# Kernel optimization log

Measured on AMD Instinct MI355X. Metric: run time of the kernel, lower is better.

The kernel has to match this reference:

```python
import jax, jax.numpy as jnp
import numpy as np

B, N, S, D, K = 8, 8192, 2048, 256, 3
MLP = [256, 128]
EPS = 1e-5


def setup_inputs() -> dict:
    key = jax.random.key(0)
    ks = jax.random.split(key, 12)
    inp = {
        "xyz1": jax.random.normal(ks[0], (B, N, 3), dtype=jnp.float32),
        "xyz2": jax.random.normal(ks[1], (B, S, 3), dtype=jnp.float32),
        "points1": jax.random.normal(ks[2], (B, N, D), dtype=jnp.float32),
        "points2": jax.random.normal(ks[3], (B, S, D), dtype=jnp.float32),
        # relation conv: Conv2d(4 -> 1, kernel 1x1) == linear over last dim
        "rel_w": jax.random.normal(ks[4], (4,), dtype=jnp.float32) * 0.5,
        "rel_b": jnp.zeros((), dtype=jnp.float32),
        # mlp layer 0: Conv1d(2D -> 256, k=1) + BN
        "W0": jax.random.normal(ks[5], (MLP[0], 2 * D), dtype=jnp.float32) * (1.0 / np.sqrt(2 * D)),
        "b0": jnp.zeros((MLP[0],), dtype=jnp.float32),
        "g0": jnp.ones((MLP[0],), dtype=jnp.float32),
        "be0": jnp.zeros((MLP[0],), dtype=jnp.float32),
        # mlp layer 1: Conv1d(256 -> 128, k=1) + BN
        "W1": jax.random.normal(ks[6], (MLP[1], MLP[0]), dtype=jnp.float32) * (1.0 / np.sqrt(MLP[0])),
        "b1": jnp.zeros((MLP[1],), dtype=jnp.float32),
        "g1": jnp.ones((MLP[1],), dtype=jnp.float32),
        "be1": jnp.zeros((MLP[1],), dtype=jnp.float32),
    }
    return inp


def _gather(points, idx):
    # points: [B,S,C], idx: [B,N,K] -> [B,N,K,C]
    return jax.vmap(lambda p, i: p[i])(points, idx)


def _bn_relu(x, gamma, beta):
    # training-mode BatchNorm1d over [B,N,C]: stats over (B,N), biased var
    mean = jnp.mean(x, axis=(0, 1))
    var = jnp.var(x, axis=(0, 1))
    xn = (x - mean) * jax.lax.rsqrt(var + EPS)
    return jax.nn.relu(xn * gamma + beta)


def reference(xyz1, xyz2, points1, points2, rel_w, rel_b,
              W0, b0, g0, be0, W1, b1, g1, be1):
    # pairwise squared distances [B,N,S]
    d = (jnp.sum(xyz1 ** 2, -1)[:, :, None]
         + jnp.sum(xyz2 ** 2, -1)[:, None, :]
         - 2.0 * jnp.einsum('bnc,bmc->bnm', xyz1, xyz2))
    neg_d, idx = jax.lax.top_k(-d, K)          # K smallest distances
    dists = -neg_d                              # [B,N,K]

    offset = xyz1[:, :, None, :] - _gather(xyz2, idx)        # [B,N,K,3]
    rel = jnp.concatenate([dists[..., None], offset], -1)    # [B,N,K,4]
    weight = jax.nn.sigmoid(rel @ rel_w + rel_b)              # [B,N,K]

    interp = jnp.mean(_gather(points2, idx) * weight[..., None], axis=2)  # [B,N,D]
    h = jnp.concatenate([points1, interp], axis=-1)           # [B,N,2D]

    h = _bn_relu(jnp.einsum('bnc,oc->bno', h, W0) + b0, g0, be0)
    h = _bn_relu(jnp.einsum('bnc,oc->bno', h, W1) + b1, g1, be1)
    return h  # [B,N,128]
```

## Files before the change

### kernel.cpp

```cpp
#include <hip/hip_runtime.h>
#include <stdint.h>
#include <stddef.h>

#define B_   8
#define N_   8192
#define S_   2048
#define D_   256
#define M_   (B_*N_)
#define C0_  256
#define C1_  128
#define K2D_ 512
#define TS8_ 8
#define SEG8_ (S_/TS8_)
#define SWP_ 264

typedef __attribute__((ext_vector_type(8))) short short8;
typedef __attribute__((ext_vector_type(4))) float f32x4;
typedef __attribute__((ext_vector_type(2))) float f32x2;

__device__ __forceinline__ short f2bf(float f) {
  unsigned u = __float_as_uint(f);
  u += 0x7fffu + ((u >> 16) & 1u);
  return (short)(u >> 16);
}
__device__ __forceinline__ float bf2f(short s) {
  return __uint_as_float(((unsigned)(unsigned short)s) << 16);
}

__device__ __forceinline__ void cp16(const void* g, void* l) {
  __builtin_amdgcn_global_load_lds(
      (__attribute__((address_space(1))) void*)(g),
      (__attribute__((address_space(3))) void*)(l), 16, 0, 0);
}

__global__ void convw_kernel(const float* __restrict__ W0,
                             const float* __restrict__ W1,
                             const float* __restrict__ xyz2,
                             short* __restrict__ W0b, short* __restrict__ W1b,
                             float* __restrict__ xyz2p, float* __restrict__ stats) {
  int i = blockIdx.x * 256 + threadIdx.x;
  if (blockIdx.x == 0) {
    stats[threadIdx.x] = 0.f;
    stats[256 + threadIdx.x] = 0.f;
    stats[512 + threadIdx.x] = 0.f;
  }
  if (i < C0_ * K2D_) W0b[i] = f2bf(W0[i]);
  if (i < C1_ * C0_)  W1b[i] = f2bf(W1[i]);
  if (i < B_ * S_) {
    const int b = i >> 11, s = i & (S_ - 1);
    float x = xyz2[(size_t)i * 3 + 0];
    float y = xyz2[(size_t)i * 3 + 1];
    float z = xyz2[(size_t)i * 3 + 2];
    float ss = __fadd_rn(__fadd_rn(__fmul_rn(x, x), __fmul_rn(y, y)), __fmul_rn(z, z));
    float* xw = xyz2p + (size_t)b * 4 * S_;
    xw[s] = x; xw[S_ + s] = y; xw[2 * S_ + s] = z; xw[3 * S_ + s] = ss;
  }
}

__global__ __launch_bounds__(512, 8)
void topk_kernel(const float* __restrict__ xyz1, const float* __restrict__ xyz2p,
                 const float* __restrict__ relw, const float* __restrict__ relb,
                 int* __restrict__ idx_out, float* __restrict__ w_out) {
  __shared__ float cd[TS8_][64][3];
  __shared__ int   ci[TS8_][64][3];
  const int tid  = threadIdx.x;
  const int lane = tid & 63;
  const int seg  = __builtin_amdgcn_readfirstlane(tid >> 6);
  const int b    = blockIdx.x >> 7;
  const int n    = (blockIdx.x & 127) * 64 + lane;

  const float* p = xyz1 + ((size_t)b * N_ + n) * 3;
  const float ax = p[0], ay = p[1], az = p[2];
  const float s1 = __fadd_rn(__fadd_rn(__fmul_rn(ax, ax), __fmul_rn(ay, ay)), __fmul_rn(az, az));

  const float* xw = xyz2p + (size_t)b * 4 * S_;
  const f32x2* XP = (const f32x2*)(xw)           + seg * (SEG8_ / 2);
  const f32x2* YP = (const f32x2*)(xw + S_)      + seg * (SEG8_ / 2);
  const f32x2* ZP = (const f32x2*)(xw + 2 * S_)  + seg * (SEG8_ / 2);
  const f32x2* WP = (const f32x2*)(xw + 3 * S_)  + seg * (SEG8_ / 2);

  float d0 = 3.4e38f, d1 = 3.4e38f, d2 = 3.4e38f;
  int   i0 = 0, i1 = 0, i2 = 0;
  const int sbeg = seg * SEG8_;
  {
    #pragma clang fp contract(off)
    #pragma unroll 4
    for (int pr = 0; pr < SEG8_ / 2; pr++) {
      f32x2 X = XP[pr], Y = YP[pr], Z = ZP[pr], W = WP[pr];
      f32x2 t1 = ax * X;
      f32x2 t2 = ay * Y;
      f32x2 t3 = az * Z;
      f32x2 dt = (t1 + t2) + t3;
      f32x2 e  = s1 + W;
      f32x2 m  = 2.0f * dt;
      f32x2 d  = e - m;
      const float dlo = d.x, dhi = d.y;
      if (fminf(dlo, dhi) < d2) {
        const int s = sbeg + 2 * pr;
        if (dlo < d2) {
          if (dlo < d1) {
            d2 = d1; i2 = i1;
            if (dlo < d0) { d1 = d0; i1 = i0; d0 = dlo; i0 = s; }
            else          { d1 = dlo; i1 = s; }
          } else { d2 = dlo; i2 = s; }
        }
        if (dhi < d2) {
          if (dhi < d1) {
            d2 = d1; i2 = i1;
            if (dhi < d0) { d1 = d0; i1 = i0; d0 = dhi; i0 = s + 1; }
            else          { d1 = dhi; i1 = s + 1; }
          } else { d2 = dhi; i2 = s + 1; }
        }
      }
    }
  }
  cd[seg][lane][0] = d0; cd[seg][lane][1] = d1; cd[seg][lane][2] = d2;
  ci[seg][lane][0] = i0; ci[seg][lane][1] = i1; ci[seg][lane][2] = i2;
  __syncthreads();

  if (tid < 64) {
    float m0 = 3.4e38f, m1 = 3.4e38f, m2 = 3.4e38f;
    int   j0 = 0, j1 = 0, j2 = 0;
    #pragma unroll
    for (int sg = 0; sg < TS8_; sg++) {
      #pragma unroll
      for (int k = 0; k < 3; k++) {
        float d = cd[sg][tid][k];
        int   ix = ci[sg][tid][k];
        if (d < m2) {
          if (d < m1) {
            m2 = m1; j2 = j1;
            if (d < m0) { m1 = m0; j1 = j0; m0 = d; j0 = ix; }
            else        { m1 = d;  j1 = ix; }
          } else { m2 = d; j2 = ix; }
        }
      }
    }
    const float w0r = relw[0], w1r = relw[1], w2r = relw[2], w3r = relw[3], br = relb[0];
    const size_t base = ((size_t)b * N_ + n) * 3;
    float dd[3] = {m0, m1, m2};
    int   ii[3] = {j0, j1, j2};
    #pragma unroll
    for (int k = 0; k < 3; k++) {
      const int s = ii[k];
      float ox = ax - xw[s], oy = ay - xw[S_ + s], oz = az - xw[2 * S_ + s];
      float t = dd[k] * w0r + ox * w1r + oy * w2r + oz * w3r + br;
      float w = 1.0f / (1.0f + expf(-t));
      idx_out[base + k] = s;
      w_out[base + k] = w * (1.0f / 3.0f);
    }
  }
}

__global__ __launch_bounds__(256, 2)
void gemm1_kernel(const float* __restrict__ p1, const float* __restrict__ p2,
                  const int* __restrict__ idx, const float* __restrict__ wts,
                  const short* __restrict__ Bw, const float* __restrict__ bias,
                  short* __restrict__ Cb, float* __restrict__ stats) {
  __shared__ __align__(16) short sA[128 * 32];
  __shared__ __align__(16) short sB[2][256 * 32];
  const int tid = threadIdx.x;
  const int lane = tid & 63;
  const int wave = tid >> 6;
  const int wm = wave & 1;
  const int wn = wave >> 1;
  const size_t mbase = (size_t)blockIdx.x * 128;
  const int lrow = lane >> 2;
  const int lcol = (lane & 3) * 8;

  int rowg[2]; int ia[2][3]; float wa[2][3]; const float* pbase[2];
  #pragma unroll
  for (int t = 0; t < 2; t++) {
    const int row = (int)mbase + wave * 32 + t * 16 + lrow;
    rowg[t] = row;
    pbase[t] = p2 + (size_t)(row >> 13) * S_ * D_;
    ia[t][0] = idx[row * 3 + 0]; ia[t][1] = idx[row * 3 + 1]; ia[t][2] = idx[row * 3 + 2];
    wa[t][0] = wts[row * 3 + 0]; wa[t][1] = wts[row * 3 + 1]; wa[t][2] = wts[row * 3 + 2];
  }

  f32x4 acc[4][8] = {};
  float4 v[2][6];

  #define LOAD_A(K0)                                                          \
    if ((K0) < D_) {                                                          \
      _Pragma("unroll")                                                       \
      for (int t = 0; t < 2; t++) {                                           \
        const float* src = p1 + (size_t)rowg[t] * D_ + (K0) + lcol;           \
        v[t][0] = *(const float4*)src; v[t][1] = *(const float4*)(src + 4);   \
      }                                                                       \
    } else {                                                                  \
      const int c2 = (K0) - D_ + lcol;                                        \
      _Pragma("unroll")                                                       \
      for (int t = 0; t < 2; t++) {                                           \
        const float* q0 = pbase[t] + (size_t)ia[t][0] * D_ + c2;              \
        const float* q1 = pbase[t] + (size_t)ia[t][1] * D_ + c2;              \
        const float* q2 = pbase[t] + (size_t)ia[t][2] * D_ + c2;              \
        v[t][0] = *(const float4*)q0; v[t][1] = *(const float4*)(q0 + 4);     \
        v[t][2] = *(const float4*)q1; v[t][3] = *(const float4*)(q1 + 4);     \
        v[t][4] = *(const float4*)q2; v[t][5] = *(const float4*)(q2 + 4);     \
      }                                                                       \
    }

  #define STAGE_B(K0, BUF)                                                    \
    _Pragma("unroll")                                                         \
    for (int t = 0; t < 4; t++) {                                             \
      const int r = wave * 64 + t * 16;                                       \
      cp16(Bw + (size_t)(r + lrow) * K2D_ + (K0) + lcol, &sB[BUF][r * 32]);   \
    }

  LOAD_A(0);
  STAGE_B(0, 0);

  for (int k0 = 0, it = 0; k0 < K2D_; k0 += 32, it++) {
    #pragma unroll
    for (int t = 0; t < 2; t++) {
      const int r = wave * 32 + t * 16;
      float fv[8];
      if (k0 < D_) {
        fv[0] = v[t][0].x; fv[1] = v[t][0].y; fv[2] = v[t][0].z; fv[3] = v[t][0].w;
        fv[4] = v[t][1].x; fv[5] = v[t][1].y; fv[6] = v[t][1].z; fv[7] = v[t][1].w;
      } else {
        fv[0] = wa[t][0] * v[t][0].x + wa[t][1] * v[t][2].x + wa[t][2] * v[t][4].x;
        fv[1] = wa[t][0] * v[t][0].y + wa[t][1] * v[t][2].y + wa[t][2] * v[t][4].y;
        fv[2] = wa[t][0] * v[t][0].z + wa[t][1] * v[t][2].z + wa[t][2] * v[t][4].z;
        fv[3] = wa[t][0] * v[t][0].w + wa[t][1] * v[t][2].w + wa[t][2] * v[t][4].w;
        fv[4] = wa[t][0] * v[t][1].x + wa[t][1] * v[t][3].x + wa[t][2] * v[t][5].x;
        fv[5] = wa[t][0] * v[t][1].y + wa[t][1] * v[t][3].y + wa[t][2] * v[t][5].y;
        fv[6] = wa[t][0] * v[t][1].z + wa[t][1] * v[t][3].z + wa[t][2] * v[t][5].z;
        fv[7] = wa[t][0] * v[t][1].w + wa[t][1] * v[t][3].w + wa[t][2] * v[t][5].w;
      }
      short8 o;
      #pragma unroll
      for (int e = 0; e < 8; e++) o[e] = f2bf(fv[e]);
      *(short8*)&sA[(r + lrow) * 32 + lcol] = o;
    }
    __syncthreads();

    const int kn = k0 + 32;
    if (kn < K2D_) {
      STAGE_B(kn, (it + 1) & 1);
      LOAD_A(kn);
    }

    const int mr = lane & 15;
    const int ks = (lane >> 4) * 8;
    short8 af[4], bfr[8];
    #pragma unroll
    for (int i = 0; i < 4; i++) af[i]  = *(const short8*)&sA[(wm * 64 + i * 16 + mr) * 32 + ks];
    #pragma unroll
    for (int j = 0; j < 8; j++) bfr[j] = *(const short8*)&sB[it & 1][(wn * 128 + j * 16 + mr) * 32 + ks];
    #pragma unroll
    for (int i = 0; i < 4; i++)
      #pragma unroll
      for (int j = 0; j < 8; j++)
        acc[i][j] = __builtin_amdgcn_mfma_f32_16x16x32_bf16(af[i], bfr[j], acc[i][j], 0, 0, 0);
    __syncthreads();
  }
  #undef LOAD_A
  #undef STAGE_B

  const int cr = (lane >> 4) * 4;
  const int cc = lane & 15;
  float ps[8], ps2[8];
  #pragma unroll
  for (int j = 0; j < 8; j++) {
    const int col = wn * 128 + j * 16 + cc;
    const float bv = bias[col];
    float s = 0.f, s2 = 0.f;
    #pragma unroll
    for (int i = 0; i < 4; i++) {
      #pragma unroll
      for (int r = 0; r < 4; r++) {
        const float vv = acc[i][j][r];
        s += vv; s2 += vv * vv;
        const size_t row = mbase + wm * 64 + i * 16 + cr + r;
        Cb[row * C0_ + col] = f2bf(vv + bv);
      }
    }
    ps[j] = s; ps2[j] = s2;
  }
  #pragma unroll
  for (int j = 0; j < 8; j++) {
    ps[j]  += __shfl_xor(ps[j], 16);  ps[j]  += __shfl_xor(ps[j], 32);
    ps2[j] += __shfl_xor(ps2[j], 16); ps2[j] += __shfl_xor(ps2[j], 32);
  }
  float* sred = (float*)sA;
  if (wm == 1 && lane < 16) {
    #pragma unroll
    for (int j = 0; j < 8; j++) {
      const int c = wn * 128 + j * 16 + lane;
      sred[2 * c] = ps[j]; sred[2 * c + 1] = ps2[j];
    }
  }
  __syncthreads();
  if (wm == 0 && lane < 16) {
    #pragma unroll
    for (int j = 0; j < 8; j++) {
      const int c = wn * 128 + j * 16 + lane;
      atomicAdd(&stats[c],       ps[j]  + sred[2 * c]);
      atomicAdd(&stats[C0_ + c], ps2[j] + sred[2 * c + 1]);
    }
  }
}

__global__ __launch_bounds__(256, 2)
void gemm2_kernel(const short* __restrict__ A, const short* __restrict__ Bw,
                  const float* __restrict__ ssn, const float* __restrict__ bias,
                  short* __restrict__ Cb, float* __restrict__ stats) {
  __shared__ __align__(16) short sW[C1_ * SWP_];
  __shared__ float sred[3 * 256];
  const int tid = threadIdx.x;
  const int lane = tid & 63;
  const int wave = tid >> 6;
  const size_t mbase = (size_t)blockIdx.x * 128;

  #pragma unroll
  for (int i = 0; i < 16; i++) {
    const int flat = i * 256 + tid;
    const int n = flat >> 5;
    const int kb = flat & 31;
    *(short8*)&sW[n * SWP_ + kb * 8] = *(const short8*)(Bw + (size_t)flat * 8);
  }
  __syncthreads();

  f32x4 acc[2][8] = {};
  const int mr = lane & 15;
  const int ksq = (lane >> 4) * 8;

  for (int k0 = 0; k0 < C0_; k0 += 32) {
    const int kk = k0 + ksq;
    float4 sc0 = *(const float4*)(ssn + kk);
    float4 sc1 = *(const float4*)(ssn + kk + 4);
    float4 sh0 = *(const float4*)(ssn + C0_ + kk);
    float4 sh1 = *(const float4*)(ssn + C0_ + kk + 4);
    const float sc[8] = {sc0.x, sc0.y, sc0.z, sc0.w, sc1.x, sc1.y, sc1.z, sc1.w};
    const float sh[8] = {sh0.x, sh0.y, sh0.z, sh0.w, sh1.x, sh1.y, sh1.z, sh1.w};
    short8 af[2];
    #pragma unroll
    for (int i = 0; i < 2; i++) {
      const size_t row = mbase + wave * 32 + i * 16 + mr;
      short8 av = *(const short8*)(A + row * C0_ + kk);
      short8 o;
      #pragma unroll
      for (int e = 0; e < 8; e++) {
        float f = bf2f(av[e]) * sc[e] + sh[e];
        o[e] = f2bf(f > 0.f ? f : 0.f);
      }
      af[i] = o;
    }
    short8 bf8[8];
    #pragma unroll
    for (int j = 0; j < 8; j++) bf8[j] = *(const short8*)&sW[(j * 16 + mr) * SWP_ + kk];
    #pragma unroll
    for (int i = 0; i < 2; i++)
      #pragma unroll
      for (int j = 0; j < 8; j++)
        acc[i][j] = __builtin_amdgcn_mfma_f32_16x16x32_bf16(af[i], bf8[j], acc[i][j], 0, 0, 0);
  }

  const int cr = (lane >> 4) * 4;
  const int cc = lane & 15;
  float ps[8], ps2[8];
  #pragma unroll
  for (int j = 0; j < 8; j++) {
    const int col = j * 16 + cc;
    const float bv = bias[col];
    float s = 0.f, s2 = 0.f;
    #pragma unroll
    for (int i = 0; i < 2; i++) {
      #pragma unroll
      for (int r = 0; r < 4; r++) {
        const float vv = acc[i][j][r];
        s += vv; s2 += vv * vv;
        const size_t row = mbase + wave * 32 + i * 16 + cr + r;
        Cb[row * C1_ + col] = f2bf(vv + bv);
      }
    }
    ps[j] = s; ps2[j] = s2;
  }
  #pragma unroll
  for (int j = 0; j < 8; j++) {
    ps[j]  += __shfl_xor(ps[j], 16);  ps[j]  += __shfl_xor(ps[j], 32);
    ps2[j] += __shfl_xor(ps2[j], 16); ps2[j] += __shfl_xor(ps2[j], 32);
  }
  if (wave > 0 && lane < 16) {
    #pragma unroll
    for (int j = 0; j < 8; j++) {
      const int c = j * 16 + lane;
      sred[(wave - 1) * 256 + c]       = ps[j];
      sred[(wave - 1) * 256 + 128 + c] = ps2[j];
    }
  }
  __syncthreads();
  if (wave == 0 && lane < 16) {
    #pragma unroll
    for (int j = 0; j < 8; j++) {
      const int c = j * 16 + lane;
      float s  = ps[j]  + sred[c]       + sred[256 + c]       + sred[512 + c];
      float s2 = ps2[j] + sred[128 + c] + sred[256 + 128 + c] + sred[512 + 128 + c];
      atomicAdd(&stats[c],       s);
      atomicAdd(&stats[C1_ + c], s2);
    }
  }
}

__global__ void stats_final_kernel(const float* __restrict__ stats, const int C,
                                   const float* __restrict__ bias,
                                   const float* __restrict__ g, const float* __restrict__ be,
                                   float* __restrict__ ss) {
  const int c = threadIdx.x;
  if (c >= C) return;
  const float inv = 1.0f / (float)M_;
  float m0 = stats[c] * inv;
  float var = stats[C + c] * inv - m0 * m0;
  float mean = m0 + bias[c];
  float sc = g[c] * rsqrtf(var + 1e-5f);
  ss[c] = sc;
  ss[C + c] = be[c] - mean * sc;
}

__global__ __launch_bounds__(256, 1)
void norm2_kernel(const short* __restrict__ a2, const float* __restrict__ ss,
                  float* __restrict__ out) {
  const size_t t = (size_t)blockIdx.x * 256 + threadIdx.x;
  const size_t base = t * 8;
  const int c = (int)(base & (C1_ - 1));
  short8 v8 = *(const short8*)(a2 + base);
  float vv[8];
  #pragma unroll
  for (int k = 0; k < 8; k++) {
    float v = bf2f(v8[k]) * ss[c + k] + ss[C1_ + c + k];
    vv[k] = v > 0.f ? v : 0.f;
  }
  *(float4*)(out + base)     = make_float4(vv[0], vv[1], vv[2], vv[3]);
  *(float4*)(out + base + 4) = make_float4(vv[4], vv[5], vv[6], vv[7]);
}

extern "C" void kernel_launch(void* const* d_in, const int* in_sizes, int n_in,
                              void* d_out, int out_size, void* d_ws, size_t ws_size,
                              hipStream_t stream) {
  const float* xyz1 = (const float*)d_in[0];
  const float* xyz2 = (const float*)d_in[1];
  const float* pts1 = (const float*)d_in[2];
  const float* pts2 = (const float*)d_in[3];
  const float* relw = (const float*)d_in[4];
  const float* relb = (const float*)d_in[5];
  const float* W0   = (const float*)d_in[6];
  const float* b0   = (const float*)d_in[7];
  const float* g0   = (const float*)d_in[8];
  const float* be0  = (const float*)d_in[9];
  const float* W1   = (const float*)d_in[10];
  const float* b1   = (const float*)d_in[11];
  const float* g1   = (const float*)d_in[12];
  const float* be1  = (const float*)d_in[13];

  char* ws = (char*)d_ws;
  constexpr size_t IDX_OFF = 0;
  constexpr size_t WTS_OFF = IDX_OFF + (size_t)M_ * 3 * 4;
  constexpr size_t W0B_OFF = WTS_OFF + (size_t)M_ * 3 * 4;
  constexpr size_t W1B_OFF = W0B_OFF + (size_t)C0_ * K2D_ * 2;
  constexpr size_t XW_OFF  = W1B_OFF + (size_t)C1_ * C0_ * 2;
  constexpr size_t A1_OFF  = XW_OFF + (size_t)B_ * 4 * S_ * 4;
  constexpr size_t A2_OFF  = A1_OFF + (size_t)M_ * C0_ * 2;
  constexpr size_t ST_OFF  = A2_OFF + (size_t)M_ * C1_ * 2;
  constexpr size_t SS1_OFF = ST_OFF + (size_t)768 * 4;
  constexpr size_t SS2_OFF = SS1_OFF + (size_t)2 * C0_ * 4;

  int*   idx   = (int*)(ws + IDX_OFF);
  float* wts   = (float*)(ws + WTS_OFF);
  short* W0b   = (short*)(ws + W0B_OFF);
  short* W1b   = (short*)(ws + W1B_OFF);
  float* xyz2p = (float*)(ws + XW_OFF);
  short* a1    = (short*)(ws + A1_OFF);
  short* a2    = (short*)(ws + A2_OFF);
  float* st    = (float*)(ws + ST_OFF);
  float* ss1   = (float*)(ws + SS1_OFF);
  float* ss2   = (float*)(ws + SS2_OFF);
  float* outp  = (float*)d_out;

  convw_kernel<<<512, 256, 0, stream>>>(W0, W1, xyz2, W0b, W1b, xyz2p, st);
  topk_kernel<<<B_ * (N_ / 64), 512, 0, stream>>>(xyz1, xyz2p, relw, relb, idx, wts);

  gemm1_kernel<<<M_ / 128, 256, 0, stream>>>(pts1, pts2, idx, wts, W0b, b0, a1, st);
  stats_final_kernel<<<1, 256, 0, stream>>>(st, C0_, b0, g0, be0, ss1);

  gemm2_kernel<<<M_ / 128, 256, 0, stream>>>(a1, W1b, ss1, b1, a2, st + 512);
  stats_final_kernel<<<1, 128, 0, stream>>>(st + 512, C1_, b1, g1, be1, ss2);
  norm2_kernel<<<(size_t)M_ * C1_ / 8 / 256, 256, 0, stream>>>(a2, ss2, outp);
}
```

Measured before the change: 292.7 us.

## Halve gemm1 M-tile to 64 rows to raise occupancy and block count

Shrinks the gemm1 block tile from 128 to 64 rows, so each thread stages a single A row-segment and each wave holds half the accumulators. The launch bound moves from 2 to 3 blocks per SM and the grid doubles. The aim is more waves in flight to hide the latency of the gathered points2 loads. The cost is that each block now reuses the 256-column B tile over only half as many rows, doubling W0 traffic, and twice as many blocks do the stats atomics.

```diff
diff --git a/kernel.cpp b/kernel.cpp
--- a/kernel.cpp
+++ b/kernel.cpp
@@ -152,53 +152,46 @@
   }
 }
 
-__global__ __launch_bounds__(256, 2)
+__global__ __launch_bounds__(256, 3)
 void gemm1_kernel(const float* __restrict__ p1, const float* __restrict__ p2,
                   const int* __restrict__ idx, const float* __restrict__ wts,
                   const short* __restrict__ Bw, const float* __restrict__ bias,
                   short* __restrict__ Cb, float* __restrict__ stats) {
-  __shared__ __align__(16) short sA[128 * 32];
+  __shared__ __align__(16) short sA[64 * 32];
   __shared__ __align__(16) short sB[2][256 * 32];
   const int tid = threadIdx.x;
   const int lane = tid & 63;
   const int wave = tid >> 6;
   const int wm = wave & 1;
   const int wn = wave >> 1;
-  const size_t mbase = (size_t)blockIdx.x * 128;
+  const size_t mbase = (size_t)blockIdx.x * 64;
   const int lrow = lane >> 2;
   const int lcol = (lane & 3) * 8;
 
-  int rowg[2]; int ia[2][3]; float wa[2][3]; const float* pbase[2];
-  #pragma unroll
-  for (int t = 0; t < 2; t++) {
-    const int row = (int)mbase + wave * 32 + t * 16 + lrow;
-    rowg[t] = row;
-    pbase[t] = p2 + (size_t)(row >> 13) * S_ * D_;
-    ia[t][0] = idx[row * 3 + 0]; ia[t][1] = idx[row * 3 + 1]; ia[t][2] = idx[row * 3 + 2];
-    wa[t][0] = wts[row * 3 + 0]; wa[t][1] = wts[row * 3 + 1]; wa[t][2] = wts[row * 3 + 2];
-  }
-
-  f32x4 acc[4][8] = {};
-  float4 v[2][6];
+  const int srow = tid >> 2;
+  const int scol = (tid & 3) * 8;
+  const int grow = (int)mbase + srow;
+  const float* p1r = p1 + (size_t)grow * D_ + scol;
+  const float* pb  = p2 + (size_t)(grow >> 13) * S_ * D_ + scol;
+  const float* q0a = pb + (size_t)idx[grow * 3 + 0] * D_;
+  const float* q1a = pb + (size_t)idx[grow * 3 + 1] * D_;
+  const float* q2a = pb + (size_t)idx[grow * 3 + 2] * D_;
+  const float w0a = wts[grow * 3 + 0];
+  const float w1a = wts[grow * 3 + 1];
+  const float w2a = wts[grow * 3 + 2];
+
+  f32x4 acc[2][8] = {};
+  float4 v[6];
 
   #define LOAD_A(K0)                                                          \
     if ((K0) < D_) {                                                          \
-      _Pragma("unroll")                                                       \
-      for (int t = 0; t < 2; t++) {                                           \
-        const float* src = p1 + (size_t)rowg[t] * D_ + (K0) + lcol;           \
-        v[t][0] = *(const float4*)src; v[t][1] = *(const float4*)(src + 4);   \
-      }                                                                       \
+      v[0] = *(const float4*)(p1r + (K0));                                    \
+      v[1] = *(const float4*)(p1r + (K0) + 4);                                \
     } else {                                                                  \
-      const int c2 = (K0) - D_ + lcol;                                        \
-      _Pragma("unroll")                                                       \
-      for (int t = 0; t < 2; t++) {                                           \
-        const float* q0 = pbase[t] + (size_t)ia[t][0] * D_ + c2;              \
-        const float* q1 = pbase[t] + (size_t)ia[t][1] * D_ + c2;              \
-        const float* q2 = pbase[t] + (size_t)ia[t][2] * D_ + c2;              \
-        v[t][0] = *(const float4*)q0; v[t][1] = *(const float4*)(q0 + 4);     \
-        v[t][2] = *(const float4*)q1; v[t][3] = *(const float4*)(q1 + 4);     \
-        v[t][4] = *(const float4*)q2; v[t][5] = *(const float4*)(q2 + 4);     \
-      }                                                                       \
+      const int c2 = (K0) - D_;                                               \
+      v[0] = *(const float4*)(q0a + c2); v[1] = *(const float4*)(q0a + c2 + 4);\
+      v[2] = *(const float4*)(q1a + c2); v[3] = *(const float4*)(q1a + c2 + 4);\
+      v[4] = *(const float4*)(q2a + c2); v[5] = *(const float4*)(q2a + c2 + 4);\
     }
 
   #define STAGE_B(K0, BUF)                                                    \
@@ -212,27 +205,25 @@
   STAGE_B(0, 0);
 
   for (int k0 = 0, it = 0; k0 < K2D_; k0 += 32, it++) {
-    #pragma unroll
-    for (int t = 0; t < 2; t++) {
-      const int r = wave * 32 + t * 16;
+    {
       float fv[8];
       if (k0 < D_) {
-        fv[0] = v[t][0].x; fv[1] = v[t][0].y; fv[2] = v[t][0].z; fv[3] = v[t][0].w;
-        fv[4] = v[t][1].x; fv[5] = v[t][1].y; fv[6] = v[t][1].z; fv[7] = v[t][1].w;
+        fv[0] = v[0].x; fv[1] = v[0].y; fv[2] = v[0].z; fv[3] = v[0].w;
+        fv[4] = v[1].x; fv[5] = v[1].y; fv[6] = v[1].z; fv[7] = v[1].w;
       } else {
-        fv[0] = wa[t][0] * v[t][0].x + wa[t][1] * v[t][2].x + wa[t][2] * v[t][4].x;
-        fv[1] = wa[t][0] * v[t][0].y + wa[t][1] * v[t][2].y + wa[t][2] * v[t][4].y;
-        fv[2] = wa[t][0] * v[t][0].z + wa[t][1] * v[t][2].z + wa[t][2] * v[t][4].z;
-        fv[3] = wa[t][0] * v[t][0].w + wa[t][1] * v[t][2].w + wa[t][2] * v[t][4].w;
-        fv[4] = wa[t][0] * v[t][1].x + wa[t][1] * v[t][3].x + wa[t][2] * v[t][5].x;
-        fv[5] = wa[t][0] * v[t][1].y + wa[t][1] * v[t][3].y + wa[t][2] * v[t][5].y;
-        fv[6] = wa[t][0] * v[t][1].z + wa[t][1] * v[t][3].z + wa[t][2] * v[t][5].z;
-        fv[7] = wa[t][0] * v[t][1].w + wa[t][1] * v[t][3].w + wa[t][2] * v[t][5].w;
+        fv[0] = w0a * v[0].x + w1a * v[2].x + w2a * v[4].x;
+        fv[1] = w0a * v[0].y + w1a * v[2].y + w2a * v[4].y;
+        fv[2] = w0a * v[0].z + w1a * v[2].z + w2a * v[4].z;
+        fv[3] = w0a * v[0].w + w1a * v[2].w + w2a * v[4].w;
+        fv[4] = w0a * v[1].x + w1a * v[3].x + w2a * v[5].x;
+        fv[5] = w0a * v[1].y + w1a * v[3].y + w2a * v[5].y;
+        fv[6] = w0a * v[1].z + w1a * v[3].z + w2a * v[5].z;
+        fv[7] = w0a * v[1].w + w1a * v[3].w + w2a * v[5].w;
       }
       short8 o;
       #pragma unroll
       for (int e = 0; e < 8; e++) o[e] = f2bf(fv[e]);
-      *(short8*)&sA[(r + lrow) * 32 + lcol] = o;
+      *(short8*)&sA[srow * 32 + scol] = o;
     }
     __syncthreads();
 
@@ -244,13 +235,13 @@
 
     const int mr = lane & 15;
     const int ks = (lane >> 4) * 8;
-    short8 af[4], bfr[8];
-    #pragma unroll
-    for (int i = 0; i < 4; i++) af[i]  = *(const short8*)&sA[(wm * 64 + i * 16 + mr) * 32 + ks];
+    short8 af[2], bfr[8];
+    #pragma unroll
+    for (int i = 0; i < 2; i++) af[i]  = *(const short8*)&sA[(wm * 32 + i * 16 + mr) * 32 + ks];
     #pragma unroll
     for (int j = 0; j < 8; j++) bfr[j] = *(const short8*)&sB[it & 1][(wn * 128 + j * 16 + mr) * 32 + ks];
     #pragma unroll
-    for (int i = 0; i < 4; i++)
+    for (int i = 0; i < 2; i++)
       #pragma unroll
       for (int j = 0; j < 8; j++)
         acc[i][j] = __builtin_amdgcn_mfma_f32_16x16x32_bf16(af[i], bfr[j], acc[i][j], 0, 0, 0);
@@ -268,12 +259,12 @@
     const float bv = bias[col];
     float s = 0.f, s2 = 0.f;
     #pragma unroll
-    for (int i = 0; i < 4; i++) {
+    for (int i = 0; i < 2; i++) {
       #pragma unroll
       for (int r = 0; r < 4; r++) {
         const float vv = acc[i][j][r];
         s += vv; s2 += vv * vv;
-        const size_t row = mbase + wm * 64 + i * 16 + cr + r;
+        const size_t row = mbase + wm * 32 + i * 16 + cr + r;
         Cb[row * C0_ + col] = f2bf(vv + bv);
       }
     }
@@ -481,7 +472,7 @@
   convw_kernel<<<512, 256, 0, stream>>>(W0, W1, xyz2, W0b, W1b, xyz2p, st);
   topk_kernel<<<B_ * (N_ / 64), 512, 0, stream>>>(xyz1, xyz2p, relw, relb, idx, wts);
 
-  gemm1_kernel<<<M_ / 128, 256, 0, stream>>>(pts1, pts2, idx, wts, W0b, b0, a1, st);
+  gemm1_kernel<<<M_ / 64, 256, 0, stream>>>(pts1, pts2, idx, wts, W0b, b0, a1, st);
   stats_final_kernel<<<1, 256, 0, stream>>>(st, C0_, b0, g0, be0, ss1);
 
   gemm2_kernel<<<M_ / 128, 256, 0, stream>>>(a1, W1b, ss1, b1, a2, st + 512);
```

New measurement: 298.3 us. No clear change (+1.9%).

## Split gather-interpolation into separate kernel and stream bf16 A via async copies

Applied to the files above, without the earlier changes.

Removes the in-GEMM gather, weighted interpolation and bf16 conversion of the A operand. A new interp_kernel writes the concatenated [points1, interp] activations as a bf16 buffer, and gemm1 double-buffers both A and B tiles with async global-to-LDS copies under a single barrier per iteration. It also swizzles block-to-row mapping across batches. The trade is an extra 64 MB write/read round trip through HBM plus another launch, in exchange for a simpler, better-pipelined GEMM mainloop.

```diff
diff --git a/kernel.cpp b/kernel.cpp
--- a/kernel.cpp
+++ b/kernel.cpp
@@ -152,112 +152,102 @@
   }
 }
 
+__global__ __launch_bounds__(256, 8)
+void interp_kernel(const float* __restrict__ p1, const float* __restrict__ p2,
+                   const int* __restrict__ idx, const float* __restrict__ wts,
+                   short* __restrict__ h) {
+  const int tid = threadIdx.x;
+  const int seg = tid & 63;
+  const size_t row = (size_t)(blockIdx.x & 7) * (M_ / 8)
+                   + (size_t)(blockIdx.x >> 3) * 4 + (tid >> 6);
+  short8 o;
+  if (seg < 32) {
+    const float* src = p1 + row * D_ + seg * 8;
+    const float4 a = *(const float4*)src;
+    const float4 b = *(const float4*)(src + 4);
+    o[0] = f2bf(a.x); o[1] = f2bf(a.y); o[2] = f2bf(a.z); o[3] = f2bf(a.w);
+    o[4] = f2bf(b.x); o[5] = f2bf(b.y); o[6] = f2bf(b.z); o[7] = f2bf(b.w);
+    *(short8*)&h[row * K2D_ + seg * 8] = o;
+  } else {
+    const int c = (seg - 32) * 8;
+    const int i0 = idx[row * 3 + 0], i1 = idx[row * 3 + 1], i2 = idx[row * 3 + 2];
+    const float w0 = wts[row * 3 + 0], w1 = wts[row * 3 + 1], w2 = wts[row * 3 + 2];
+    const float* pb = p2 + (row >> 13) * ((size_t)S_ * D_) + c;
+    const float* q0 = pb + (size_t)i0 * D_;
+    const float* q1 = pb + (size_t)i1 * D_;
+    const float* q2 = pb + (size_t)i2 * D_;
+    const float4 a0 = *(const float4*)q0, b0 = *(const float4*)(q0 + 4);
+    const float4 a1 = *(const float4*)q1, b1 = *(const float4*)(q1 + 4);
+    const float4 a2 = *(const float4*)q2, b2 = *(const float4*)(q2 + 4);
+    float fv[8];
+    fv[0] = w0 * a0.x + w1 * a1.x + w2 * a2.x;
+    fv[1] = w0 * a0.y + w1 * a1.y + w2 * a2.y;
+    fv[2] = w0 * a0.z + w1 * a1.z + w2 * a2.z;
+    fv[3] = w0 * a0.w + w1 * a1.w + w2 * a2.w;
+    fv[4] = w0 * b0.x + w1 * b1.x + w2 * b2.x;
+    fv[5] = w0 * b0.y + w1 * b1.y + w2 * b2.y;
+    fv[6] = w0 * b0.z + w1 * b1.z + w2 * b2.z;
+    fv[7] = w0 * b0.w + w1 * b1.w + w2 * b2.w;
+    #pragma unroll
+    for (int e = 0; e < 8; e++) o[e] = f2bf(fv[e]);
+    *(short8*)&h[row * K2D_ + D_ + c] = o;
+  }
+}
+
 __global__ __launch_bounds__(256, 2)
-void gemm1_kernel(const float* __restrict__ p1, const float* __restrict__ p2,
-                  const int* __restrict__ idx, const float* __restrict__ wts,
-                  const short* __restrict__ Bw, const float* __restrict__ bias,
+void gemm1_kernel(const short* __restrict__ h, const short* __restrict__ Bw,
+                  const float* __restrict__ bias,
                   short* __restrict__ Cb, float* __restrict__ stats) {
-  __shared__ __align__(16) short sA[128 * 32];
+  __shared__ __align__(16) short sA[2][128 * 32];
   __shared__ __align__(16) short sB[2][256 * 32];
   const int tid = threadIdx.x;
   const int lane = tid & 63;
   const int wave = tid >> 6;
   const int wm = wave & 1;
   const int wn = wave >> 1;
-  const size_t mbase = (size_t)blockIdx.x * 128;
-  const int lrow = lane >> 2;
-  const int lcol = (lane & 3) * 8;
-
-  int rowg[2]; int ia[2][3]; float wa[2][3]; const float* pbase[2];
-  #pragma unroll
-  for (int t = 0; t < 2; t++) {
-    const int row = (int)mbase + wave * 32 + t * 16 + lrow;
-    rowg[t] = row;
-    pbase[t] = p2 + (size_t)(row >> 13) * S_ * D_;
-    ia[t][0] = idx[row * 3 + 0]; ia[t][1] = idx[row * 3 + 1]; ia[t][2] = idx[row * 3 + 2];
-    wa[t][0] = wts[row * 3 + 0]; wa[t][1] = wts[row * 3 + 1]; wa[t][2] = wts[row * 3 + 2];
-  }
-
-  f32x4 acc[4][8] = {};
-  float4 v[2][6];
-
-  #define LOAD_A(K0)                                                          \
-    if ((K0) < D_) {                                                          \
-      _Pragma("unroll")                                                       \
-      for (int t = 0; t < 2; t++) {                                           \
-        const float* src = p1 + (size_t)rowg[t] * D_ + (K0) + lcol;           \
-        v[t][0] = *(const float4*)src; v[t][1] = *(const float4*)(src + 4);   \
-      }                                                                       \
-    } else {                                                                  \
-      const int c2 = (K0) - D_ + lcol;                                        \
-      _Pragma("unroll")                                                       \
-      for (int t = 0; t < 2; t++) {                                           \
-        const float* q0 = pbase[t] + (size_t)ia[t][0] * D_ + c2;              \
-        const float* q1 = pbase[t] + (size_t)ia[t][1] * D_ + c2;              \
-        const float* q2 = pbase[t] + (size_t)ia[t][2] * D_ + c2;              \
-        v[t][0] = *(const float4*)q0; v[t][1] = *(const float4*)(q0 + 4);     \
-        v[t][2] = *(const float4*)q1; v[t][3] = *(const float4*)(q1 + 4);     \
-        v[t][4] = *(const float4*)q2; v[t][5] = *(const float4*)(q2 + 4);     \
-      }                                                                       \
-    }
-
-  #define STAGE_B(K0, BUF)                                                    \
+  const size_t mbase = (size_t)(blockIdx.x & 7) * (M_ / 8)
+                     + (size_t)(blockIdx.x >> 3) * 128;
+
+  #define STAGE(K0, BUF)                                                      \
+    _Pragma("unroll")                                                         \
+    for (int t = 0; t < 2; t++) {                                             \
+      const int ca = wave * 128 + t * 64 + lane;                              \
+      cp16(h + (mbase + (ca >> 2)) * K2D_ + (K0) + (ca & 3) * 8,              \
+           &sA[BUF][(wave * 128 + t * 64) * 8]);                              \
+    }                                                                         \
     _Pragma("unroll")                                                         \
     for (int t = 0; t < 4; t++) {                                             \
-      const int r = wave * 64 + t * 16;                                       \
-      cp16(Bw + (size_t)(r + lrow) * K2D_ + (K0) + lcol, &sB[BUF][r * 32]);   \
-    }
-
-  LOAD_A(0);
-  STAGE_B(0, 0);
+      const int cb = wave * 256 + t * 64 + lane;                              \
+      cp16(Bw + (size_t)(cb >> 2) * K2D_ + (K0) + (cb & 3) * 8,               \
+           &sB[BUF][(wave * 256 + t * 64) * 8]);                              \
+    }
+
+  f32x4 acc[4][8] = {};
+  STAGE(0, 0);
+
+  const int mr = lane & 15;
+  const int ks = (lane >> 4) * 8;
 
   for (int k0 = 0, it = 0; k0 < K2D_; k0 += 32, it++) {
-    #pragma unroll
-    for (int t = 0; t < 2; t++) {
-      const int r = wave * 32 + t * 16;
-      float fv[8];
-      if (k0 < D_) {
-        fv[0] = v[t][0].x; fv[1] = v[t][0].y; fv[2] = v[t][0].z; fv[3] = v[t][0].w;
-        fv[4] = v[t][1].x; fv[5] = v[t][1].y; fv[6] = v[t][1].z; fv[7] = v[t][1].w;
-      } else {
-        fv[0] = wa[t][0] * v[t][0].x + wa[t][1] * v[t][2].x + wa[t][2] * v[t][4].x;
-        fv[1] = wa[t][0] * v[t][0].y + wa[t][1] * v[t][2].y + wa[t][2] * v[t][4].y;
-        fv[2] = wa[t][0] * v[t][0].z + wa[t][1] * v[t][2].z + wa[t][2] * v[t][4].z;
-        fv[3] = wa[t][0] * v[t][0].w + wa[t][1] * v[t][2].w + wa[t][2] * v[t][4].w;
-        fv[4] = wa[t][0] * v[t][1].x + wa[t][1] * v[t][3].x + wa[t][2] * v[t][5].x;
-        fv[5] = wa[t][0] * v[t][1].y + wa[t][1] * v[t][3].y + wa[t][2] * v[t][5].y;
-        fv[6] = wa[t][0] * v[t][1].z + wa[t][1] * v[t][3].z + wa[t][2] * v[t][5].z;
-        fv[7] = wa[t][0] * v[t][1].w + wa[t][1] * v[t][3].w + wa[t][2] * v[t][5].w;
-      }
-      short8 o;
-      #pragma unroll
-      for (int e = 0; e < 8; e++) o[e] = f2bf(fv[e]);
-      *(short8*)&sA[(r + lrow) * 32 + lcol] = o;
-    }
     __syncthreads();
-
     const int kn = k0 + 32;
-    if (kn < K2D_) {
-      STAGE_B(kn, (it + 1) & 1);
-      LOAD_A(kn);
-    }
-
-    const int mr = lane & 15;
-    const int ks = (lane >> 4) * 8;
+    if (kn < K2D_) STAGE(kn, (it + 1) & 1);
+
     short8 af[4], bfr[8];
     #pragma unroll
-    for (int i = 0; i < 4; i++) af[i]  = *(const short8*)&sA[(wm * 64 + i * 16 + mr) * 32 + ks];
-    #pragma unroll
-    for (int j = 0; j < 8; j++) bfr[j] = *(const short8*)&sB[it & 1][(wn * 128 + j * 16 + mr) * 32 + ks];
+    for (int i = 0; i < 4; i++)
+      af[i]  = *(const short8*)&sA[it & 1][(wm * 64 + i * 16 + mr) * 32 + ks];
+    #pragma unroll
+    for (int j = 0; j < 8; j++)
+      bfr[j] = *(const short8*)&sB[it & 1][(wn * 128 + j * 16 + mr) * 32 + ks];
     #pragma unroll
     for (int i = 0; i < 4; i++)
       #pragma unroll
       for (int j = 0; j < 8; j++)
         acc[i][j] = __builtin_amdgcn_mfma_f32_16x16x32_bf16(af[i], bfr[j], acc[i][j], 0, 0, 0);
-    __syncthreads();
-  }
-  #undef LOAD_A
-  #undef STAGE_B
+  }
+  #undef STAGE
+  __syncthreads();
 
   const int cr = (lane >> 4) * 4;
   const int cc = lane & 15;
@@ -460,7 +450,8 @@
   constexpr size_t W0B_OFF = WTS_OFF + (size_t)M_ * 3 * 4;
   constexpr size_t W1B_OFF = W0B_OFF + (size_t)C0_ * K2D_ * 2;
   constexpr size_t XW_OFF  = W1B_OFF + (size_t)C1_ * C0_ * 2;
-  constexpr size_t A1_OFF  = XW_OFF + (size_t)B_ * 4 * S_ * 4;
+  constexpr size_t H_OFF   = XW_OFF + (size_t)B_ * 4 * S_ * 4;
+  constexpr size_t A1_OFF  = H_OFF + (size_t)M_ * K2D_ * 2;
   constexpr size_t A2_OFF  = A1_OFF + (size_t)M_ * C0_ * 2;
   constexpr size_t ST_OFF  = A2_OFF + (size_t)M_ * C1_ * 2;
   constexpr size_t SS1_OFF = ST_OFF + (size_t)768 * 4;
@@ -471,6 +462,7 @@
   short* W0b   = (short*)(ws + W0B_OFF);
   short* W1b   = (short*)(ws + W1B_OFF);
   float* xyz2p = (float*)(ws + XW_OFF);
+  short* h     = (short*)(ws + H_OFF);
   short* a1    = (short*)(ws + A1_OFF);
   short* a2    = (short*)(ws + A2_OFF);
   float* st    = (float*)(ws + ST_OFF);
@@ -481,7 +473,8 @@
   convw_kernel<<<512, 256, 0, stream>>>(W0, W1, xyz2, W0b, W1b, xyz2p, st);
   topk_kernel<<<B_ * (N_ / 64), 512, 0, stream>>>(xyz1, xyz2p, relw, relb, idx, wts);
 
-  gemm1_kernel<<<M_ / 128, 256, 0, stream>>>(pts1, pts2, idx, wts, W0b, b0, a1, st);
+  interp_kernel<<<M_ * 64 / 256, 256, 0, stream>>>(pts1, pts2, idx, wts, h);
+  gemm1_kernel<<<M_ / 128, 256, 0, stream>>>(h, W0b, b0, a1, st);
   stats_final_kernel<<<1, 256, 0, stream>>>(st, C0_, b0, g0, be0, ss1);
 
   gemm2_kernel<<<M_ / 128, 256, 0, stream>>>(a1, W1b, ss1, b1, a2, st + 512);
```

Measured after the change: 320.1 us. 1.09x slower.
